# Kernel tuning notes

Hardware: AMD Instinct MI355X
Metric: run time of the kernel (lower is better)

The kernel has to match this reference:

```python
import jax, jax.numpy as jnp
import numpy as np

NQ = 14            # qubits = ceil(log2(16384))
DIM = 2 ** NQ
OUT = 1000         # out_features (slice last OUT probs)


def _apply_ry(state, theta, axis):
    """Apply RY(theta) on the qubit at `axis` of state shaped (B, 2,...,2).
    RY = [[cos(t/2), -sin(t/2)], [sin(t/2), cos(t/2)]] (real)."""
    c = jnp.cos(theta / 2)
    s = jnp.sin(theta / 2)
    x = jnp.moveaxis(state, axis, -1)
    x0, x1 = x[..., 0], x[..., 1]
    y = jnp.stack([c * x0 - s * x1, s * x0 + c * x1], axis=-1)
    return jnp.moveaxis(y, -1, axis)


def _apply_cz(state, axis):
    """CZ on adjacent qubits (axis, axis+1): flip sign of |11> amplitudes."""
    sign = jnp.ones((2, 2), state.dtype).at[1, 1].set(-1.0)
    shape = [1] * state.ndim
    shape[axis] = 2
    shape[axis + 1] = 2
    return state * sign.reshape(shape)


def _circuit(inp, weights, bias):
    B, F = inp.shape
    # AmplitudeEmbedding(pad_with=1, normalize=True)
    if F < DIM:
        inp = jnp.pad(inp, ((0, 0), (0, DIM - F)), constant_values=1.0)
    norm = jnp.sqrt(jnp.sum(inp * inp, axis=1, keepdims=True))
    state = (inp / norm).reshape((B,) + (2,) * NQ)
    # SimplifiedTwoDesign: initial RY layer (bias)
    for w in range(NQ):
        state = _apply_ry(state, bias[w], 1 + w)
    # entangling layers: even CZ/RY block then odd CZ/RY block
    nlayer = weights.shape[0]
    for l in range(nlayer):
        for start in (0, 1):
            for i in range(start, NQ - 1, 2):
                state = _apply_cz(state, 1 + i)
                state = _apply_ry(state, weights[l, i, 0], 1 + i)
                state = _apply_ry(state, weights[l, i, 1], 1 + i + 1)
    amps = state.reshape(B, DIM)
    probs = amps * amps  # real statevector -> |amp|^2
    return probs[:, -OUT:]


def setup_inputs() -> dict:
    key = jax.random.key(0)
    k1, k2, k3 = jax.random.split(key, 3)
    return {
        "input": jax.random.normal(k1, (512, 16384), dtype=jnp.float32),
        "weights": jax.random.normal(k2, (2, NQ - 1, 2), dtype=jnp.float32),
        "bias": jax.random.normal(k3, (NQ,), dtype=jnp.float32),
    }


def reference(input, weights, bias):
    return _circuit(input, weights, bias)
```

## Files before the change

### kernel.cpp

```cpp
#include <hip/hip_runtime.h>

#define NQ 14
#define DIM 16384
#define OUT_N 1000
#define PRUNED 2048

using v2f = __attribute__((ext_vector_type(2))) float;

__host__ __device__ constexpr int WI(int l, int i, int k) {
    return 14 + (l * 13 + i) * 2 + k;
}

__device__ __forceinline__ int swzB(int a) { return a ^ ((a >> 5) & 31); }

template<int B, int NP>
__device__ __forceinline__ void ry(v2f* x, float c, float s) {
    if constexpr (B == 0) {
#pragma unroll
        for (int p = 0; p < NP; ++p) {
            float a0 = x[p].x, a1 = x[p].y;
            x[p].x = c * a0 - s * a1;
            x[p].y = s * a0 + c * a1;
        }
    } else {
        constexpr int pb = B - 1;
#pragma unroll
        for (int m = 0; m < NP / 2; ++m) {
            int p0 = ((m >> pb) << (pb + 1)) | (m & ((1 << pb) - 1));
            int p1 = p0 | (1 << pb);
            v2f lo = x[p0], hi = x[p1];
            x[p0] = lo * c - hi * s;
            x[p1] = hi * c + lo * s;
        }
    }
}

template<int BH, int BL, int NP>
__device__ __forceinline__ void cz(v2f* x) {
    static_assert(BH > BL, "");
    if constexpr (BL >= 1) {
#pragma unroll
        for (int p = 0; p < NP; ++p)
            if (((p >> (BH - 1)) & 1) && ((p >> (BL - 1)) & 1)) x[p] = -x[p];
    } else {
#pragma unroll
        for (int p = 0; p < NP; ++p)
            if ((p >> (BH - 1)) & 1) x[p].y = -x[p].y;
    }
}

#define BLK(BH, I0, I1, NP)                                       \
    cz<BH, BH - 1, NP>(x);                                        \
    { float2 cc = csl[I0]; ry<BH, NP>(x, cc.x, cc.y); }           \
    { float2 cd = csl[I1]; ry<BH - 1, NP>(x, cd.x, cd.y); }

__global__ __launch_bounds__(256, 2)
void qnn_fused2(const float* __restrict__ in, const float* __restrict__ wts,
                const float* __restrict__ bias, float* __restrict__ out) {
    __shared__ float lds[PRUNED];
    __shared__ float2 csl[66];
    __shared__ float red[4];

    const int t = threadIdx.x;
    const int b = blockIdx.x;

    if (t < 66) {
        float th = (t < NQ) ? bias[t] : wts[t - NQ];
        csl[t] = make_float2(cosf(0.5f * th), sinf(0.5f * th));
    }

    const float* __restrict__ xin = in + (size_t)b * DIM;
    v2f x[32];
#pragma unroll
    for (int p = 0; p < 32; ++p) {
        x[p].x = xin[((2 * p) << 8) | t];
        x[p].y = xin[((2 * p + 1) << 8) | t];
    }

    float pp = 0.f;
#pragma unroll
    for (int p = 0; p < 32; ++p) pp = fmaf(x[p].x, x[p].x, fmaf(x[p].y, x[p].y, pp));
#pragma unroll
    for (int d = 32; d; d >>= 1) pp += __shfl_xor(pp, d);
    if ((t & 63) == 0) red[t >> 6] = pp;
    __syncthreads();
    const float scale = 1.0f / sqrtf(red[0] + red[1] + red[2] + red[3]);

    { float2 cc;
      cc = csl[0]; ry<5, 32>(x, cc.x, cc.y);
      cc = csl[1]; ry<4, 32>(x, cc.x, cc.y);
      cc = csl[2]; ry<3, 32>(x, cc.x, cc.y);
      cc = csl[3]; ry<2, 32>(x, cc.x, cc.y);
      cc = csl[4]; ry<1, 32>(x, cc.x, cc.y);
      cc = csl[5]; ry<0, 32>(x, cc.x, cc.y); }
    BLK(5, WI(0,0,0), WI(0,0,1), 32)
    BLK(3, WI(0,2,0), WI(0,2,1), 32)
    BLK(1, WI(0,4,0), WI(0,4,1), 32)
    BLK(4, WI(0,1,0), WI(0,1,1), 32)
    BLK(2, WI(0,3,0), WI(0,3,1), 32)
    BLK(5, WI(1,0,0), WI(1,0,1), 32)
    BLK(3, WI(1,2,0), WI(1,2,1), 32)
    BLK(4, WI(1,1,0), WI(1,1,1), 32)

#pragma unroll
    for (int p = 28; p < 32; ++p) {
        lds[swzB(((2 * p - 56) << 8) | t)] = x[p].x * scale;
        lds[swzB(((2 * p - 55) << 8) | t)] = x[p].y * scale;
    }
    __syncthreads();

    if (t < 64) {
        const int s = t;
#pragma unroll
        for (int l = 0; l < 32; ++l) {
            float v = lds[swzB((s << 5) | l)];
            if (l & 1) x[l >> 1].y = v; else x[l >> 1].x = v;
        }
        { float2 cc;
          cc = csl[9];  ry<4, 16>(x, cc.x, cc.y);
          cc = csl[10]; ry<3, 16>(x, cc.x, cc.y);
          cc = csl[11]; ry<2, 16>(x, cc.x, cc.y);
          cc = csl[12]; ry<1, 16>(x, cc.x, cc.y);
          cc = csl[13]; ry<0, 16>(x, cc.x, cc.y); }
        BLK(3, WI(0,10,0), WI(0,10,1), 16)
        BLK(1, WI(0,12,0), WI(0,12,1), 16)
        BLK(2, WI(0,11,0), WI(0,11,1), 16)
        BLK(1, WI(1,12,0), WI(1,12,1), 16)
#pragma unroll
        for (int l = 0; l < 32; ++l)
            lds[swzB((s << 5) | l)] = (l & 1) ? x[l >> 1].y : x[l >> 1].x;
    }
    __syncthreads();
    if (t < 64) {
        const int s = t;
#pragma unroll
        for (int l = 0; l < 32; ++l) {
            float v = lds[swzB(((s >> 4) << 9) | (l << 4) | (s & 15))];
            if (l & 1) x[l >> 1].y = v; else x[l >> 1].x = v;
        }
        { float2 cc;
          cc = csl[6]; ry<3, 16>(x, cc.x, cc.y);
          cc = csl[7]; ry<2, 16>(x, cc.x, cc.y);
          cc = csl[8]; ry<1, 16>(x, cc.x, cc.y); }
        BLK(3, WI(0,6,0), WI(0,6,1), 16)
        BLK(1, WI(0,8,0), WI(0,8,1), 16)
        BLK(4, WI(0,5,0), WI(0,5,1), 16)
        BLK(2, WI(0,7,0), WI(0,7,1), 16)
        BLK(3, WI(1,6,0), WI(1,6,1), 16)
#pragma unroll
        for (int l = 0; l < 32; ++l)
            lds[swzB(((s >> 4) << 9) | (l << 4) | (s & 15))] =
                (l & 1) ? x[l >> 1].y : x[l >> 1].x;
    }
    __syncthreads();
    if (t < 64) {
        const int s = t;
#pragma unroll
        for (int l = 0; l < 32; ++l) {
            float v = lds[swzB(((s >> 2) << 7) | (l << 2) | (s & 3))];
            if (l & 1) x[l >> 1].y = v; else x[l >> 1].x = v;
        }
        BLK(2, WI(0,9,0),  WI(0,9,1),  16)
        BLK(3, WI(1,8,0),  WI(1,8,1),  16)
        BLK(1, WI(1,10,0), WI(1,10,1), 16)
        BLK(4, WI(1,7,0),  WI(1,7,1),  16)
        BLK(2, WI(1,9,0),  WI(1,9,1),  16)
#pragma unroll
        for (int l = 0; l < 32; ++l)
            lds[swzB(((s >> 2) << 7) | (l << 2) | (s & 3))] =
                (l & 1) ? x[l >> 1].y : x[l >> 1].x;
    }
    __syncthreads();
    if (t < 64) {
        const int s = t;
#pragma unroll
        for (int l = 0; l < 32; ++l) {
            float v = lds[swzB((l << 6) | s)];
            if (l & 1) x[l >> 1].y = v; else x[l >> 1].x = v;
        }
        BLK(3, WI(1,4,0), WI(1,4,1), 16)
        BLK(4, WI(1,3,0), WI(1,3,1), 16)
        BLK(2, WI(1,5,0), WI(1,5,1), 16)
#pragma unroll
        for (int l = 0; l < 32; ++l)
            lds[swzB((l << 6) | s)] = (l & 1) ? x[l >> 1].y : x[l >> 1].x;
    }
    __syncthreads();
    if (t < 64) {
        const int s = t;
#pragma unroll
        for (int l = 0; l < 32; ++l) {
            float v = lds[swzB((s << 5) | l)];
            if (l & 1) x[l >> 1].y = v; else x[l >> 1].x = v;
        }
        BLK(2, WI(1,11,0), WI(1,11,1), 16)

        if (s >= 32) {
            float* __restrict__ orow = out + (size_t)b * OUT_N;
            const int base = s * 32 - 1048;
#pragma unroll
            for (int l = 0; l < 32; ++l) {
                int j = base + l;
                float v = (l & 1) ? x[l >> 1].y : x[l >> 1].x;
                if (j >= 0) orow[j] = v * v;
            }
        }
    }
}

extern "C" void kernel_launch(void* const* d_in, const int* in_sizes, int n_in,
                              void* d_out, int out_size, void* d_ws, size_t ws_size,
                              hipStream_t stream) {
    const float* in   = (const float*)d_in[0];
    const float* wts  = (const float*)d_in[1];
    const float* bias = (const float*)d_in[2];
    float* out = (float*)d_out;

    const int nb = in_sizes[0] / DIM;
    qnn_fused2<<<nb, 256, 0, stream>>>(in, wts, bias, out);
}
```

Measured before the change: 90.38 us.

## Process two batch rows per 512-thread block with separate LDS buffers

Each block now handles two rows: two 256-thread halves load and transform their own row, and the serial single-wave tail stages run on two waves at once, one per row, each using its own LDS buffer. This halves the grid to 256 blocks and puts twice the work into each single-wave stage. The grid of 256 blocks on a 256-CU part leaves one block per CU and lowers the number of blocks in flight. The 512-thread launch bound with 64 live float2 registers per thread may also increase register pressure.

```diff
diff --git a/kernel.cpp b/kernel.cpp
--- a/kernel.cpp
+++ b/kernel.cpp
@@ -54,15 +54,19 @@
     { float2 cc = csl[I0]; ry<BH, NP>(x, cc.x, cc.y); }           \
     { float2 cd = csl[I1]; ry<BH - 1, NP>(x, cd.x, cd.y); }
 
-__global__ __launch_bounds__(256, 2)
-void qnn_fused2(const float* __restrict__ in, const float* __restrict__ wts,
-                const float* __restrict__ bias, float* __restrict__ out) {
-    __shared__ float lds[PRUNED];
+__global__ __launch_bounds__(512, 2)
+void qnn_fused3(const float* __restrict__ in, const float* __restrict__ wts,
+                const float* __restrict__ bias, float* __restrict__ out,
+                int nrows) {
+    __shared__ float lds[2 * PRUNED];
     __shared__ float2 csl[66];
-    __shared__ float red[4];
+    __shared__ float red[8];
 
     const int t = threadIdx.x;
-    const int b = blockIdx.x;
+    const int half = t >> 8;
+    const int tt = t & 255;
+    const int brow = blockIdx.x * 2 + half;
+    const int b = (brow < nrows) ? brow : (nrows - 1);
 
     if (t < 66) {
         float th = (t < NQ) ? bias[t] : wts[t - NQ];
@@ -73,8 +77,8 @@
     v2f x[32];
 #pragma unroll
     for (int p = 0; p < 32; ++p) {
-        x[p].x = xin[((2 * p) << 8) | t];
-        x[p].y = xin[((2 * p + 1) << 8) | t];
+        x[p].x = xin[((2 * p) << 8) | tt];
+        x[p].y = xin[((2 * p + 1) << 8) | tt];
     }
 
     float pp = 0.f;
@@ -84,7 +88,8 @@
     for (int d = 32; d; d >>= 1) pp += __shfl_xor(pp, d);
     if ((t & 63) == 0) red[t >> 6] = pp;
     __syncthreads();
-    const float scale = 1.0f / sqrtf(red[0] + red[1] + red[2] + red[3]);
+    const float scale = 1.0f / sqrtf(red[4 * half + 0] + red[4 * half + 1] +
+                                     red[4 * half + 2] + red[4 * half + 3]);
 
     { float2 cc;
       cc = csl[0]; ry<5, 32>(x, cc.x, cc.y);
@@ -102,18 +107,22 @@
     BLK(3, WI(1,2,0), WI(1,2,1), 32)
     BLK(4, WI(1,1,0), WI(1,1,1), 32)
 
-#pragma unroll
-    for (int p = 28; p < 32; ++p) {
-        lds[swzB(((2 * p - 56) << 8) | t)] = x[p].x * scale;
-        lds[swzB(((2 * p - 55) << 8) | t)] = x[p].y * scale;
-    }
-    __syncthreads();
-
-    if (t < 64) {
-        const int s = t;
-#pragma unroll
-        for (int l = 0; l < 32; ++l) {
-            float v = lds[swzB((s << 5) | l)];
+    {
+        float* __restrict__ pb = lds + half * PRUNED;
+#pragma unroll
+        for (int p = 28; p < 32; ++p) {
+            pb[swzB(((2 * p - 56) << 8) | tt)] = x[p].x * scale;
+            pb[swzB(((2 * p - 55) << 8) | tt)] = x[p].y * scale;
+        }
+    }
+    __syncthreads();
+
+    if (t < 128) {
+        const int s = t & 63;
+        float* __restrict__ buf = lds + (t >> 6) * PRUNED;
+#pragma unroll
+        for (int l = 0; l < 32; ++l) {
+            float v = buf[swzB((s << 5) | l)];
             if (l & 1) x[l >> 1].y = v; else x[l >> 1].x = v;
         }
         { float2 cc;
@@ -128,14 +137,15 @@
         BLK(1, WI(1,12,0), WI(1,12,1), 16)
 #pragma unroll
         for (int l = 0; l < 32; ++l)
-            lds[swzB((s << 5) | l)] = (l & 1) ? x[l >> 1].y : x[l >> 1].x;
-    }
-    __syncthreads();
-    if (t < 64) {
-        const int s = t;
-#pragma unroll
-        for (int l = 0; l < 32; ++l) {
-            float v = lds[swzB(((s >> 4) << 9) | (l << 4) | (s & 15))];
+            buf[swzB((s << 5) | l)] = (l & 1) ? x[l >> 1].y : x[l >> 1].x;
+    }
+    __syncthreads();
+    if (t < 128) {
+        const int s = t & 63;
+        float* __restrict__ buf = lds + (t >> 6) * PRUNED;
+#pragma unroll
+        for (int l = 0; l < 32; ++l) {
+            float v = buf[swzB(((s >> 4) << 9) | (l << 4) | (s & 15))];
             if (l & 1) x[l >> 1].y = v; else x[l >> 1].x = v;
         }
         { float2 cc;
@@ -149,15 +159,16 @@
         BLK(3, WI(1,6,0), WI(1,6,1), 16)
 #pragma unroll
         for (int l = 0; l < 32; ++l)
-            lds[swzB(((s >> 4) << 9) | (l << 4) | (s & 15))] =
+            buf[swzB(((s >> 4) << 9) | (l << 4) | (s & 15))] =
                 (l & 1) ? x[l >> 1].y : x[l >> 1].x;
     }
     __syncthreads();
-    if (t < 64) {
-        const int s = t;
-#pragma unroll
-        for (int l = 0; l < 32; ++l) {
-            float v = lds[swzB(((s >> 2) << 7) | (l << 2) | (s & 3))];
+    if (t < 128) {
+        const int s = t & 63;
+        float* __restrict__ buf = lds + (t >> 6) * PRUNED;
+#pragma unroll
+        for (int l = 0; l < 32; ++l) {
+            float v = buf[swzB(((s >> 2) << 7) | (l << 2) | (s & 3))];
             if (l & 1) x[l >> 1].y = v; else x[l >> 1].x = v;
         }
         BLK(2, WI(0,9,0),  WI(0,9,1),  16)
@@ -167,15 +178,16 @@
         BLK(2, WI(1,9,0),  WI(1,9,1),  16)
 #pragma unroll
         for (int l = 0; l < 32; ++l)
-            lds[swzB(((s >> 2) << 7) | (l << 2) | (s & 3))] =
+            buf[swzB(((s >> 2) << 7) | (l << 2) | (s & 3))] =
                 (l & 1) ? x[l >> 1].y : x[l >> 1].x;
     }
     __syncthreads();
-    if (t < 64) {
-        const int s = t;
-#pragma unroll
-        for (int l = 0; l < 32; ++l) {
-            float v = lds[swzB((l << 6) | s)];
+    if (t < 128) {
+        const int s = t & 63;
+        float* __restrict__ buf = lds + (t >> 6) * PRUNED;
+#pragma unroll
+        for (int l = 0; l < 32; ++l) {
+            float v = buf[swzB((l << 6) | s)];
             if (l & 1) x[l >> 1].y = v; else x[l >> 1].x = v;
         }
         BLK(3, WI(1,4,0), WI(1,4,1), 16)
@@ -183,20 +195,23 @@
         BLK(2, WI(1,5,0), WI(1,5,1), 16)
 #pragma unroll
         for (int l = 0; l < 32; ++l)
-            lds[swzB((l << 6) | s)] = (l & 1) ? x[l >> 1].y : x[l >> 1].x;
-    }
-    __syncthreads();
-    if (t < 64) {
-        const int s = t;
-#pragma unroll
-        for (int l = 0; l < 32; ++l) {
-            float v = lds[swzB((s << 5) | l)];
+            buf[swzB((l << 6) | s)] = (l & 1) ? x[l >> 1].y : x[l >> 1].x;
+    }
+    __syncthreads();
+    if (t < 128) {
+        const int s = t & 63;
+        const int w = t >> 6;
+        float* __restrict__ buf = lds + w * PRUNED;
+#pragma unroll
+        for (int l = 0; l < 32; ++l) {
+            float v = buf[swzB((s << 5) | l)];
             if (l & 1) x[l >> 1].y = v; else x[l >> 1].x = v;
         }
         BLK(2, WI(1,11,0), WI(1,11,1), 16)
 
-        if (s >= 32) {
-            float* __restrict__ orow = out + (size_t)b * OUT_N;
+        const int rb = blockIdx.x * 2 + w;
+        if (s >= 32 && rb < nrows) {
+            float* __restrict__ orow = out + (size_t)rb * OUT_N;
             const int base = s * 32 - 1048;
 #pragma unroll
             for (int l = 0; l < 32; ++l) {
@@ -217,5 +232,6 @@
     float* out = (float*)d_out;
 
     const int nb = in_sizes[0] / DIM;
-    qnn_fused2<<<nb, 256, 0, stream>>>(in, wts, bias, out);
-}
+    const int grid = (nb + 1) / 2;
+    qnn_fused3<<<grid, 512, 0, stream>>>(in, wts, bias, out, nb);
+}
```

New measurement: 89.49 us. No clear change (-1.0%).
